# Performance work log

Hardware: AMD Instinct MI355X
Metric: run time of the kernel (lower is better)

## Reference

```python
import jax, jax.numpy as jnp
import numpy as np

DT_MIN, DT_MAX = 1e-3, 0.1
DT_RANK, D_STATE, D_CONV = 64, 16, 4


def setup_inputs() -> dict:
    key = jax.random.key(0)
    ks = jax.random.split(key, 8)
    B, T, Dm = 4, 4096, 1024
    Dn = 2 * Dm  # expand * d_model
    s = lambda k, shape, scale=0.02: (jax.random.normal(k, shape, jnp.float32) * scale)
    return {
        "x": jax.random.normal(ks[0], (B, T, Dm), jnp.float32),
        "W_in": s(ks[1], (2 * Dn, Dm)),
        "conv_w": s(ks[2], (Dn, 1, D_CONV), 0.1),
        "conv_b": jnp.zeros((Dn,), jnp.float32),
        "W_x": s(ks[3], (DT_RANK + 2 * D_STATE, Dn)),
        "W_dt": s(ks[4], (Dn, DT_RANK)),
        "b_dt": jnp.zeros((Dn,), jnp.float32),
        "log_A": jax.random.uniform(ks[5], (Dn, D_STATE), jnp.float32),
        "D_param": jnp.ones((Dn,), jnp.float32),
        "W_out": s(ks[6], (Dm, Dn)),
        "ln_w": jnp.ones((Dm,), jnp.float32),
        "ln_b": jnp.zeros((Dm,), jnp.float32),
    }


def reference(x, W_in, conv_w, conv_b, W_x, W_dt, b_dt, log_A, D_param, W_out, ln_w, ln_b):
    B, T, Dm = x.shape
    Dn = W_dt.shape[0]
    residual = x
    # LayerNorm (biased variance, eps=1e-5, as torch)
    mu = x.mean(-1, keepdims=True)
    var = x.var(-1, keepdims=True)
    xn = (x - mu) / jnp.sqrt(var + 1e-5) * ln_w + ln_b
    # in_proj -> split into x_inner, z
    xz = xn @ W_in.T  # (B,T,2*Dn)
    x_inner, z = jnp.split(xz, 2, axis=-1)
    # causal depthwise conv (torch pads both sides d_conv-1 then slices [:T] == left-pad only)
    xc = jnp.transpose(x_inner, (0, 2, 1))  # (B,Dn,T)
    xc = jax.lax.conv_general_dilated(
        xc, conv_w, window_strides=(1,), padding=[(D_CONV - 1, 0)],
        dimension_numbers=("NCH", "OIH", "NCH"), feature_group_count=Dn)
    xc = xc + conv_b[None, :, None]
    u = jax.nn.silu(jnp.transpose(xc, (0, 2, 1)))  # (B,T,Dn)
    # input-dependent dt, B, C
    xbc = u @ W_x.T
    dt_low, B_ssm, C_ssm = jnp.split(xbc, [DT_RANK, DT_RANK + D_STATE], axis=-1)
    dt = jax.nn.softplus(dt_low @ W_dt.T + b_dt) + DT_MIN
    dt = jnp.clip(dt, DT_MIN, DT_MAX)  # (B,T,Dn)
    A = -jnp.exp(log_A)  # (Dn,N), always negative -> stable
    # selective scan: h_t = exp(dt*A)*h_{t-1} + (dt*u)*B_t ; y_t = <C_t, h_t>
    def step(h, inp):
        dt_t, u_t, B_t, C_t = inp  # (B,Dn),(B,Dn),(B,N),(B,N)
        dA = jnp.exp(dt_t[:, :, None] * A)  # (B,Dn,N)
        h = dA * h + (dt_t * u_t)[:, :, None] * B_t[:, None, :]
        y = jnp.einsum("bdn,bn->bd", h, C_t)
        return h, y

    h0 = jnp.zeros((B, Dn, D_STATE), x.dtype)
    _, ys = jax.lax.scan(
        step, h0,
        (jnp.moveaxis(dt, 1, 0), jnp.moveaxis(u, 1, 0),
         jnp.moveaxis(B_ssm, 1, 0), jnp.moveaxis(C_ssm, 1, 0)))
    y = jnp.moveaxis(ys, 0, 1)  # (B,T,Dn)
    y = y + u * D_param
    y = y * jax.nn.silu(z)
    return y @ W_out.T + residual
```

## Files before the change

kernel.cpp:

```cpp
#include <hip/hip_runtime.h>
#include <cstdint>
#include <cstddef>

#define TT 4096
#define DM 1024
#define DN 2048
#define MROWS 16384
#define NCH 64
#define CHL 64
#define SW 16
#define XBCS 128

typedef unsigned short u16;
typedef u16 ushort8_t __attribute__((ext_vector_type(8)));
typedef u16 ushort4_t __attribute__((ext_vector_type(4)));
typedef short bf16x8 __attribute__((ext_vector_type(8)));
typedef float f32x4 __attribute__((ext_vector_type(4)));

#define EXP2(x) __builtin_amdgcn_exp2f(x)
#define L2E 1.44269504f

__device__ __forceinline__ float bf2f(u16 b) {
  return __uint_as_float(((unsigned int)b) << 16);
}
__device__ __forceinline__ u16 f2bf(float f) {
  unsigned int u = __float_as_uint(f);
  u = u + 0x7FFFu + ((u >> 16) & 1u);
  return (u16)(u >> 16);
}
__device__ __forceinline__ u16 f2h(float f) {
  _Float16 h = (_Float16)f;
  return __builtin_bit_cast(u16, h);
}
__device__ __forceinline__ float h2f(u16 v) {
  return (float)__builtin_bit_cast(_Float16, v);
}

__device__ __forceinline__ void gload_lds16(const void* g, void* l) {
  __builtin_amdgcn_global_load_lds(
      (const __attribute__((address_space(1))) unsigned int*)g,
      (__attribute__((address_space(3))) unsigned int*)l, 16, 0, 0);
}

#define FENCE() asm volatile("" ::: "memory")

__global__ __launch_bounds__(256) void cvt_weights_kernel(
    const float* __restrict__ W_in, u16* __restrict__ W_in_b,
    const float* __restrict__ W_x, u16* __restrict__ W_x_b,
    const float* __restrict__ W_dt, u16* __restrict__ W_dt_b,
    const float* __restrict__ W_out, u16* __restrict__ W_out_b) {
  int b = blockIdx.x, t = threadIdx.x;
  if (b < 4096) {
    int i = b * 256 + t;
    float4 v = ((const float4*)W_in)[i];
    ushort4_t o; o[0] = f2bf(v.x); o[1] = f2bf(v.y); o[2] = f2bf(v.z); o[3] = f2bf(v.w);
    ((ushort4_t*)W_in_b)[i] = o;
  } else if (b < 4352) {
    int i = (b - 4096) * 256 + t;
    int row = i >> 9;
    ushort4_t o;
    if (row < 96) {
      float4 v = ((const float4*)W_x)[i];
      o[0] = f2bf(v.x); o[1] = f2bf(v.y); o[2] = f2bf(v.z); o[3] = f2bf(v.w);
    } else {
      o[0] = 0; o[1] = 0; o[2] = 0; o[3] = 0;
    }
    ((ushort4_t*)W_x_b)[i] = o;
  } else if (b < 4384) {
    int i = (b - 4352) * 256 + t;
    float4 v = ((const float4*)W_dt)[i];
    ushort4_t o; o[0] = f2bf(v.x); o[1] = f2bf(v.y); o[2] = f2bf(v.z); o[3] = f2bf(v.w);
    ((ushort4_t*)W_dt_b)[i] = o;
  } else {
    int i = (b - 4384) * 256 + t;
    float4 v = ((const float4*)W_out)[i];
    ushort4_t o; o[0] = f2bf(v.x); o[1] = f2bf(v.y); o[2] = f2bf(v.z); o[3] = f2bf(v.w);
    ((ushort4_t*)W_out_b)[i] = o;
  }
}

__global__ __launch_bounds__(256) void ln_kernel(const float* __restrict__ x,
    const float* __restrict__ ln_w, const float* __restrict__ ln_b,
    u16* __restrict__ xn) {
  int row = blockIdx.x;
  int tid = threadIdx.x;
  const f32x4* xr = (const f32x4*)(x + (size_t)row * DM);
  f32x4 vv = __builtin_nontemporal_load(&xr[tid]);
  float4 v; v.x = vv[0]; v.y = vv[1]; v.z = vv[2]; v.w = vv[3];
  float s  = v.x + v.y + v.z + v.w;
  float s2 = v.x*v.x + v.y*v.y + v.z*v.z + v.w*v.w;
#pragma unroll
  for (int o = 32; o > 0; o >>= 1) { s += __shfl_down(s, o, 64); s2 += __shfl_down(s2, o, 64); }
  __shared__ float red[2][4];
  __shared__ float mv[2];
  int wid = tid >> 6, lane = tid & 63;
  if (lane == 0) { red[0][wid] = s; red[1][wid] = s2; }
  __syncthreads();
  if (tid == 0) {
    float a  = red[0][0] + red[0][1] + red[0][2] + red[0][3];
    float b2 = red[1][0] + red[1][1] + red[1][2] + red[1][3];
    float mean = a * (1.f / DM);
    float var  = b2 * (1.f / DM) - mean * mean;
    mv[0] = mean; mv[1] = rsqrtf(var + 1e-5f);
  }
  __syncthreads();
  float mean = mv[0], inv = mv[1];
  float4 w = ((const float4*)ln_w)[tid];
  float4 b = ((const float4*)ln_b)[tid];
  ushort4_t o;
  o[0] = f2bf((v.x - mean) * inv * w.x + b.x);
  o[1] = f2bf((v.y - mean) * inv * w.y + b.y);
  o[2] = f2bf((v.z - mean) * inv * w.z + b.z);
  o[3] = f2bf((v.w - mean) * inv * w.w + b.w);
  *(ushort4_t*)(xn + (size_t)row * DM + tid * 4) = o;
}

template<int MODE>
__global__ __launch_bounds__(256) void gemm_mfma_nt(
    const u16* __restrict__ A, int lda,
    const u16* __restrict__ B, int ldb,
    void* __restrict__ Cp, int ldc,
    const float* __restrict__ Res, int K,
    const float* __restrict__ bias, u16* __restrict__ dl_out) {
  __shared__ __align__(16) u16 a_s[128 * 64];
  __shared__ __align__(16) u16 b_s[128 * 64];
  const int tid = threadIdx.x;
  const int w = tid >> 6, l = tid & 63;
  const int wr = w >> 1, wc = w & 1;
  const int nbx = gridDim.x, gy = gridDim.y;
  int lin = blockIdx.y * nbx + blockIdx.x;
  int xcd = lin & 7;
  int m = lin >> 3;
  int bi, bj;
  if (gy >= 8) {
    int njx = gy >> 3;
    bi = m / njx;
    bj = xcd * njx + m % njx;
  } else {
    int cpx = (nbx * gy) >> 3;
    int swz = xcd * cpx + m;
    bi = swz % nbx; bj = swz / nbx;
  }
  const int lrow = l >> 3;
  const int scol = ((l & 7) ^ lrow) * 16;

  f32x4 acc[4][4] = {};

  const int brow = (MODE == 4) ? 0 : bj;
  const u16* Abase = A + (size_t)(bi * 128 + w * 8 + lrow) * lda;
  const u16* Bbase = B + (size_t)(brow * 128 + w * 8 + lrow) * ldb;

  int kbeg = 0, kend = K;
  if constexpr (MODE == 4) { kbeg = bj * (K >> 2); kend = kbeg + (K >> 2); }
  for (int k0 = kbeg; k0 < kend; k0 += 64) {
#pragma unroll
    for (int c = 0; c < 4; c++) {
      const char* ga = (const char*)(Abase + (size_t)(c * 32) * lda + k0) + scol;
      const char* gb = (const char*)(Bbase + (size_t)(c * 32) * ldb + k0) + scol;
      gload_lds16(ga, (char*)a_s + c * 4096 + w * 1024);
      gload_lds16(gb, (char*)b_s + c * 4096 + w * 1024);
    }
    __syncthreads();
#pragma unroll
    for (int kk = 0; kk < 2; kk++) {
      bf16x8 af[4], bfr[4];
#pragma unroll
      for (int m2 = 0; m2 < 4; m2++) {
        int fr = wr * 64 + m2 * 16 + (l & 15);
        int cb = (kk * 64 + ((l >> 4) << 4)) ^ ((fr & 7) << 4);
        af[m2] = *(const bf16x8*)((const char*)a_s + fr * 128 + cb);
      }
#pragma unroll
      for (int n = 0; n < 4; n++) {
        int fr = wc * 64 + n * 16 + (l & 15);
        int cb = (kk * 64 + ((l >> 4) << 4)) ^ ((fr & 7) << 4);
        bfr[n] = *(const bf16x8*)((const char*)b_s + fr * 128 + cb);
      }
#pragma unroll
      for (int m2 = 0; m2 < 4; m2++)
#pragma unroll
        for (int n = 0; n < 4; n++)
          acc[m2][n] = __builtin_amdgcn_mfma_f32_16x16x32_bf16(af[m2], bfr[n], acc[m2][n], 0, 0, 0);
    }
    __syncthreads();
  }
  const int col0 = ((MODE == 4) ? 0 : bj * 128) + wc * 64 + (l & 15);
  const int row0 = bi * 128 + wr * 64 + (l >> 4) * 4;
#pragma unroll
  for (int m2 = 0; m2 < 4; m2++)
#pragma unroll
    for (int n = 0; n < 4; n++) {
      int col = col0 + n * 16;
      float bv = 0.f;
      if constexpr (MODE == 3) bv = bias[col];
#pragma unroll
      for (int r = 0; r < 4; r++) {
        size_t row = (size_t)(row0 + m2 * 16 + r);
        float v = acc[m2][n][r];
        if constexpr (MODE == 0) {
          ((u16*)Cp)[row * ldc + col] = f2bf(v);
        } else if constexpr (MODE == 2) {
          v += __builtin_nontemporal_load(&Res[row * ldc + col]);
          __builtin_nontemporal_store(v, &((float*)Cp)[row * ldc + col]);
        } else if constexpr (MODE == 4) {
          ((float*)Cp)[(size_t)bj * ((size_t)MROWS * 128) + row * ldc + col] = v;
        } else {
          float s = v + bv;
          float sp = __logf(1.f + __expf(s));
          float dtv = fminf(sp + 1e-3f, 0.1f);
          ((u16*)Cp)[row * ldc + col] = f2h(dtv);
        }
      }
    }
}

__global__ __launch_bounds__(256) void xbc_merge(const float* __restrict__ p,
    float* __restrict__ xbc, u16* __restrict__ dl) {
  int i = blockIdx.x * 256 + threadIdx.x;
  const size_t PS = (size_t)MROWS * 128 / 4;
  float4 a = ((const float4*)p)[i];
  float4 b = ((const float4*)p)[i + PS];
  float4 c = ((const float4*)p)[i + 2 * PS];
  float4 d = ((const float4*)p)[i + 3 * PS];
  float4 s;
  s.x = (a.x + b.x) + (c.x + d.x);
  s.y = (a.y + b.y) + (c.y + d.y);
  s.z = (a.z + b.z) + (c.z + d.z);
  s.w = (a.w + b.w) + (c.w + d.w);
  ((float4*)xbc)[i] = s;
  int col = (i & 31) * 4;
  if (col < 64) {
    int row = i >> 5;
    ushort4_t o; o[0] = f2bf(s.x); o[1] = f2bf(s.y); o[2] = f2bf(s.z); o[3] = f2bf(s.w);
    *(ushort4_t*)(dl + (size_t)row * 64 + col) = o;
  }
}

template<int MODE>
__global__ __launch_bounds__(512) void gemm256(
    const u16* __restrict__ A, int lda,
    const u16* __restrict__ B, int ldb,
    void* __restrict__ Cp, int ldc,
    const float* __restrict__ Res, int K) {
  extern __shared__ char smem[];
  const int tid = threadIdx.x;
  const int w = tid >> 6, l = tid & 63;
  const int wm = w >> 2, wn = w & 3;
  const int nbx = gridDim.x, gy = gridDim.y;
  int lin = blockIdx.y * nbx + blockIdx.x;
  int xcd = lin & 7, mm = lin >> 3;
  int bi, bj;
  if (gy >= 8) { int njx = gy >> 3; bi = mm / njx; bj = xcd * njx + mm % njx; }
  else { int cpx = (nbx * gy) >> 3; int swz = xcd * cpx + mm; bi = swz % nbx; bj = swz / nbx; }
  const int lrow = l >> 3;
  const int scol = ((l & 7) ^ lrow) * 16;
  const int l15 = l & 15, lhi = (l >> 4) << 4;
  const u16* aRow = A + (size_t)(bi * 256 + w * 8 + lrow) * lda;
  const u16* bRow = B + (size_t)(bj * 256 + w * 8 + lrow) * ldb;
  char* As = smem;
  char* Bs = smem + 65536;

#define IS_A(s, k) gload_lds16((const char*)(aRow + (size_t)((k) * 64) * lda + (size_t)(s) * 64) + scol, \
                               As + ((((s) & 1)) << 15) + (k) * 8192 + w * 1024)
#define IS_B(s, k) gload_lds16((const char*)(bRow + (size_t)((k) * 64) * ldb + (size_t)(s) * 64) + scol, \
                               Bs + ((((s) & 1)) << 15) + (k) * 8192 + w * 1024)

  f32x4 acc[8][4] = {};
  bf16x8 bf[2][4];
  const int NT = K >> 6;

  IS_B(0, 0); IS_B(0, 1); IS_B(0, 2); IS_B(0, 3);
  IS_A(0, 0); IS_A(0, 2); IS_A(0, 1); IS_A(0, 3);
  IS_B(1, 0); IS_B(1, 1); IS_B(1, 2); IS_B(1, 3); IS_A(1, 0);

#define MFMA8(MLO, KK) do { \
    bf16x8 a0_ = ardA(MLO, KK), a1_ = ardA((MLO) + 1, KK); \
    __builtin_amdgcn_s_setprio(1); \
    _Pragma("unroll") \
    for (int n_ = 0; n_ < 4; n_++) { \
      acc[MLO][n_]       = __builtin_amdgcn_mfma_f32_16x16x32_bf16(a0_, bf[KK][n_], acc[MLO][n_], 0, 0, 0); \
      acc[(MLO) + 1][n_] = __builtin_amdgcn_mfma_f32_16x16x32_bf16(a1_, bf[KK][n_], acc[(MLO) + 1][n_], 0, 0, 0); \
    } \
    __builtin_amdgcn_s_setprio(0); \
  } while (0)

  for (int t = 0; t < NT; ++t) {
    const char* Ab = As + ((t & 1) << 15);
    const char* Bb = Bs + ((t & 1) << 15);
    auto ardA = [&](int m, int kk) {
      int fr = wm * 128 + m * 16 + l15;
      int cb = (kk * 64 + lhi) ^ ((fr & 7) << 4);
      return *(const bf16x8*)(Ab + fr * 128 + cb);
    };
    auto ardB = [&](int n, int kk) {
      int fr = wn * 64 + n * 16 + l15;
      int cb = (kk * 64 + lhi) ^ ((fr & 7) << 4);
      return *(const bf16x8*)(Bb + fr * 128 + cb);
    };
    if (t + 1 < NT) IS_A(t + 1, 2);
    FENCE();
    asm volatile("s_waitcnt vmcnt(8)" ::: "memory");
    __builtin_amdgcn_s_barrier();
    FENCE();
    bf[0][0] = ardB(0, 0); bf[0][1] = ardB(1, 0); bf[0][2] = ardB(2, 0); bf[0][3] = ardB(3, 0);
    MFMA8(0, 0);
    if (t + 1 < NT) IS_A(t + 1, 1);
    MFMA8(2, 0);
    if (t + 1 < NT) IS_A(t + 1, 3);
    bf[1][0] = ardB(0, 1); bf[1][1] = ardB(1, 1); bf[1][2] = ardB(2, 1); bf[1][3] = ardB(3, 1);
    MFMA8(0, 1);
    FENCE();
    __builtin_amdgcn_s_barrier();
    FENCE();
    if (t + 2 < NT) IS_B(t + 2, 0);
    MFMA8(2, 1);
    if (t + 2 < NT) IS_B(t + 2, 1);
    FENCE();
    asm volatile("s_waitcnt vmcnt(10)" ::: "memory");
    __builtin_amdgcn_s_barrier();
    FENCE();
    MFMA8(4, 0);
    if (t + 2 < NT) IS_B(t + 2, 2);
    MFMA8(6, 0);
    if (t + 2 < NT) IS_B(t + 2, 3);
    MFMA8(4, 1);
    if (t + 2 < NT) IS_A(t + 2, 0);
    MFMA8(6, 1);
  }
#undef MFMA8
#undef IS_A
#undef IS_B

  const int col0 = bj * 256 + wn * 64 + l15;
  const int row0 = bi * 256 + wm * 128 + (l >> 4) * 4;
  const bool ntst = (MODE == 0) && (bj >= 8);
#pragma unroll
  for (int m = 0; m < 8; m++)
#pragma unroll
    for (int n = 0; n < 4; n++) {
      int col = col0 + n * 16;
#pragma unroll
      for (int r = 0; r < 4; r++) {
        size_t row = (size_t)(row0 + m * 16 + r);
        float v = acc[m][n][r];
        if constexpr (MODE == 0) {
          u16 bv = f2bf(v);
          if (ntst) __builtin_nontemporal_store(bv, &((u16*)Cp)[row * ldc + col]);
          else      ((u16*)Cp)[row * ldc + col] = bv;
        } else {
          v += __builtin_nontemporal_load(&Res[row * ldc + col]);
          __builtin_nontemporal_store(v, &((float*)Cp)[row * ldc + col]);
        }
      }
    }
}

__global__ __launch_bounds__(256) void conv_silu_kernel(const u16* __restrict__ xz,
    const float* __restrict__ conv_w, const float* __restrict__ conv_b,
    u16* __restrict__ u) {
  size_t gid = (size_t)blockIdx.x * 256 + threadIdx.x;
  int c = (int)(gid & 255);
  size_t i = gid >> 8;
  int t = (int)(i & (TT - 1));
  int d0 = c * 8;
  const u16* base = xz + i * 4096 + d0;
  ushort8_t r0 = *(const ushort8_t*)base;
  ushort8_t r1 = 0, r2 = 0, r3 = 0;
  if (t >= 1) r1 = *(const ushort8_t*)(base - 4096);
  if (t >= 2) r2 = *(const ushort8_t*)(base - 2 * 4096);
  if (t >= 3) r3 = *(const ushort8_t*)(base - 3 * 4096);
  float cbv[8];
  *(float4*)&cbv[0] = *(const float4*)(conv_b + d0);
  *(float4*)&cbv[4] = *(const float4*)(conv_b + d0 + 4);
  ushort8_t o;
#pragma unroll
  for (int j = 0; j < 8; j++) {
    float4 w = *(const float4*)(conv_w + (size_t)(d0 + j) * 4);
    float a = cbv[j] + w.w * bf2f(r0[j]) + w.z * bf2f(r1[j])
            + w.y * bf2f(r2[j]) + w.x * bf2f(r3[j]);
    a = a * __builtin_amdgcn_rcpf(1.f + EXP2(-a * L2E));
    o[j] = f2bf(a);
  }
  *(ushort8_t*)(u + i * 2048 + d0) = o;
}

__global__ __launch_bounds__(256) void scan_part1(u16* u_g,
    const u16* __restrict__ dt_g, const float* __restrict__ xbc,
    const float* __restrict__ log_A, const float* __restrict__ D_param,
    u16* __restrict__ hbuf, float* __restrict__ Sbuf) {
  int d0 = blockIdx.x * 128;
  int c  = blockIdx.y;
  int b  = blockIdx.z;
  int tid = threadIdx.x;
  int w = tid >> 6, l = tid & 63;
  int dl = tid >> 1, q = tid & 1, q8 = q << 3;
  int d = d0 + dl;
  __shared__ __align__(16) u16 u_s[2][SW][128];
  __shared__ __align__(16) u16 dts[2][SW][128];
  __shared__ __align__(16) float bc_s[2][SW][32];

  float A2[8];
  {
    float4 la0 = *(const float4*)(log_A + (size_t)d * 16 + q8);
    float4 la1 = *(const float4*)(log_A + (size_t)d * 16 + q8 + 4);
    A2[0] = -EXP2(la0.x * L2E) * L2E; A2[1] = -EXP2(la0.y * L2E) * L2E;
    A2[2] = -EXP2(la0.z * L2E) * L2E; A2[3] = -EXP2(la0.w * L2E) * L2E;
    A2[4] = -EXP2(la1.x * L2E) * L2E; A2[5] = -EXP2(la1.y * L2E) * L2E;
    A2[6] = -EXP2(la1.z * L2E) * L2E; A2[7] = -EXP2(la1.w * L2E) * L2E;
  }
  float Dp = D_param[d];
  float h[8] = {};
  float sdt = 0.f;
  size_t t0 = (size_t)b * TT + (size_t)c * CHL;
  const int sr = w * 4 + (l >> 4);
  const int sc = (l & 15) * 8;
  u16* up = u_g + t0 * 2048 + d;

#define P1STAGE(wnd, pb) { size_t i0_ = t0 + (size_t)(wnd) * SW;                          \
    gload_lds16(u_g  + (i0_ + sr) * 2048 + d0 + sc, (char*)u_s[pb] + w * 1024);           \
    gload_lds16(dt_g + (i0_ + sr) * 4096 + d0 + sc, (char*)dts[pb] + w * 1024);           \
    if (w < 2) gload_lds16(xbc + (i0_ + w * 8 + (l >> 3)) * XBCS + 64 + (l & 7) * 4,      \
                           (char*)bc_s[pb] + w * 1024); }

  P1STAGE(0, 0);
  for (int wnd = 0; wnd < CHL / SW; wnd++) {
    int pb = wnd & 1;
    __syncthreads();
    if (wnd + 1 < CHL / SW) P1STAGE(wnd + 1, pb ^ 1);
#pragma unroll 4
    for (int tt = 0; tt < SW; tt++) {
      float dtv = h2f(dts[pb][tt][dl]);
      float uv  = bf2f(u_s[pb][tt][dl]);
      sdt += dtv;
      float xin = dtv * uv;
      float yv = q ? 0.f : uv * Dp;
      float4 B0 = *(const float4*)&bc_s[pb][tt][q8];
      float4 B1 = *(const float4*)&bc_s[pb][tt][q8 + 4];
      float4 C0 = *(const float4*)&bc_s[pb][tt][16 + q8];
      float4 C1 = *(const float4*)&bc_s[pb][tt][16 + q8 + 4];
      h[0] = __builtin_fmaf(EXP2(dtv * A2[0]), h[0], xin * B0.x); yv = __builtin_fmaf(h[0], C0.x, yv);
      h[1] = __builtin_fmaf(EXP2(dtv * A2[1]), h[1], xin * B0.y); yv = __builtin_fmaf(h[1], C0.y, yv);
      h[2] = __builtin_fmaf(EXP2(dtv * A2[2]), h[2], xin * B0.z); yv = __builtin_fmaf(h[2], C0.z, yv);
      h[3] = __builtin_fmaf(EXP2(dtv * A2[3]), h[3], xin * B0.w); yv = __builtin_fmaf(h[3], C0.w, yv);
      h[4] = __builtin_fmaf(EXP2(dtv * A2[4]), h[4], xin * B1.x); yv = __builtin_fmaf(h[4], C1.x, yv);
      h[5] = __builtin_fmaf(EXP2(dtv * A2[5]), h[5], xin * B1.y); yv = __builtin_fmaf(h[5], C1.y, yv);
      h[6] = __builtin_fmaf(EXP2(dtv * A2[6]), h[6], xin * B1.z); yv = __builtin_fmaf(h[6], C1.z, yv);
      h[7] = __builtin_fmaf(EXP2(dtv * A2[7]), h[7], xin * B1.w); yv = __builtin_fmaf(h[7], C1.w, yv);
      yv += __shfl_xor(yv, 1, 64);
      if (q == 0) *up = f2h(yv);
      up += 2048;
    }
  }
  u16* hp = hbuf + (((size_t)b * NCH + c) * 16 + q8) * DN + d;
#pragma unroll
  for (int k = 0; k < 8; k++) hp[(size_t)k * DN] = f2h(h[k]);
  if (q == 0) Sbuf[((size_t)b * NCH + c) * DN + d] = sdt;
#undef P1STAGE
}

__global__ __launch_bounds__(256) void scan_combine(const float* __restrict__ log_A,
    const float* __restrict__ Sbuf, u16* __restrict__ hbuf) {
  int idx = blockIdx.x * 256 + threadIdx.x;
  int dd = idx & (DN - 1), n = (idx >> 11) & 15, b = idx >> 15;
  float A2 = -EXP2(log_A[(size_t)dd * 16 + n] * L2E) * L2E;
  float h = 0.f;
#pragma unroll
  for (int c = 0; c < NCH; c++) {
    size_t off = (((size_t)b * NCH + c) * 16 + n) * DN + dd;
    float hl = h2f(hbuf[off]);
    float P = EXP2(A2 * Sbuf[((size_t)b * NCH + c) * DN + dd]);
    hbuf[off] = f2h(h);
    h = hl + P * h;
  }
}

__global__ __launch_bounds__(256) void scan_part2(u16* yl,
    const u16* __restrict__ xz, const float* __restrict__ xbc,
    const u16* __restrict__ dt_g, const float* __restrict__ log_A,
    const u16* __restrict__ hbuf) {
  int d0 = blockIdx.x * 128;
  int c  = blockIdx.y;
  int b  = blockIdx.z;
  int tid = threadIdx.x;
  int w = tid >> 6, l = tid & 63;
  int dl = tid >> 1, q = tid & 1, q8 = q << 3;
  int d = d0 + dl;
  __shared__ __align__(16) u16 yls[2][SW][128];
  __shared__ __align__(16) u16 z_s[2][SW][128];
  __shared__ __align__(16) u16 dts[2][SW][128];
  __shared__ __align__(16) float c_s[2][SW][16];

  float A2[8];
  {
    float4 la0 = *(const float4*)(log_A + (size_t)d * 16 + q8);
    float4 la1 = *(const float4*)(log_A + (size_t)d * 16 + q8 + 4);
    A2[0] = -EXP2(la0.x * L2E) * L2E; A2[1] = -EXP2(la0.y * L2E) * L2E;
    A2[2] = -EXP2(la0.z * L2E) * L2E; A2[3] = -EXP2(la0.w * L2E) * L2E;
    A2[4] = -EXP2(la1.x * L2E) * L2E; A2[5] = -EXP2(la1.y * L2E) * L2E;
    A2[6] = -EXP2(la1.z * L2E) * L2E; A2[7] = -EXP2(la1.w * L2E) * L2E;
  }
  float hs[8];
  {
    const u16* hp = hbuf + (((size_t)b * NCH + c) * 16 + q8) * DN + d;
#pragma unroll
    for (int k = 0; k < 8; k++) hs[k] = h2f(hp[(size_t)k * DN]);
  }
  float cum = 0.f;
  size_t t0 = (size_t)b * TT + (size_t)c * CHL;
  const int sr = w * 4 + (l >> 4);
  const int sc = (l & 15) * 8;
  u16* ylp = yl + t0 * 2048 + d;

#define P2STAGE(wnd, pb) { size_t i0_ = t0 + (size_t)(wnd) * SW;                          \
    gload_lds16(yl   + (i0_ + sr) * 2048 + d0 + sc, (char*)yls[pb] + w * 1024);           \
    gload_lds16(xz   + (i0_ + sr) * 4096 + 2048 + d0 + sc, (char*)z_s[pb] + w * 1024);    \
    gload_lds16(dt_g + (i0_ + sr) * 4096 + d0 + sc, (char*)dts[pb] + w * 1024);           \
    if (w == 0) gload_lds16(xbc + (i0_ + (l >> 2)) * XBCS + 80 + (l & 3) * 4,             \
                            (char*)c_s[pb]); }

  P2STAGE(0, 0);
  for (int wnd = 0; wnd < CHL / SW; wnd++) {
    int pb = wnd & 1;
    __syncthreads();
    if (wnd + 1 < CHL / SW) P2STAGE(wnd + 1, pb ^ 1);
#pragma unroll 4
    for (int tt = 0; tt < SW; tt++) {
      float dtv = h2f(dts[pb][tt][dl]);
      cum += dtv;
      float4 C0 = *(const float4*)&c_s[pb][tt][q8];
      float4 C1 = *(const float4*)&c_s[pb][tt][q8 + 4];
      float yv = C0.x * (EXP2(cum * A2[0]) * hs[0]) + C0.y * (EXP2(cum * A2[1]) * hs[1])
               + C0.z * (EXP2(cum * A2[2]) * hs[2]) + C0.w * (EXP2(cum * A2[3]) * hs[3])
               + C1.x * (EXP2(cum * A2[4]) * hs[4]) + C1.y * (EXP2(cum * A2[5]) * hs[5])
               + C1.z * (EXP2(cum * A2[6]) * hs[6]) + C1.w * (EXP2(cum * A2[7]) * hs[7]);
      if (q == 0) yv += h2f(yls[pb][tt][dl]);
      yv += __shfl_xor(yv, 1, 64);
      float zv = bf2f(z_s[pb][tt][dl]);
      float sig = __builtin_amdgcn_rcpf(1.f + EXP2(-zv * L2E));
      if (q == 0) *ylp = f2bf(yv * zv * sig);
      ylp += 2048;
    }
  }
#undef P2STAGE
}

extern "C" void kernel_launch(void* const* d_in, const int* in_sizes, int n_in,
                              void* d_out, int out_size, void* d_ws, size_t ws_size,
                              hipStream_t stream) {
  const float* x       = (const float*)d_in[0];
  const float* W_in    = (const float*)d_in[1];
  const float* conv_w  = (const float*)d_in[2];
  const float* conv_b  = (const float*)d_in[3];
  const float* W_x     = (const float*)d_in[4];
  const float* W_dt    = (const float*)d_in[5];
  const float* b_dt    = (const float*)d_in[6];
  const float* log_A   = (const float*)d_in[7];
  const float* D_param = (const float*)d_in[8];
  const float* W_out   = (const float*)d_in[9];
  const float* ln_w    = (const float*)d_in[10];
  const float* ln_b    = (const float*)d_in[11];
  float* out = (float*)d_out;

  size_t need = (size_t)MROWS * 4096 * 2 + (size_t)MROWS * DN * 2 + (size_t)MROWS * 96 * 4;
  if (ws_size < need) return;
  u16*   xz  = (u16*)d_ws;
  u16*   u   = xz + (size_t)MROWS * 4096;
  u16*   W_out_b = (u16*)(u + (size_t)MROWS * DN);

  u16*   xn_b    = (u16*)d_out;
  float* xbc_p   = (float*)d_out;
  float* xbc     = (float*)d_out;
  u16*   hbuf    = (u16*)((char*)d_out + (32u << 20));
  u16*   W_in_b  = (u16*)((char*)d_out + (40u << 20));
  float* Sbuf    = (float*)((char*)d_out + (48u << 20));
  u16*   W_x_b   = (u16*)((char*)d_out + (50u << 20));
  u16*   W_dt_b  = (u16*)((char*)d_out + (50u << 20) + (512u << 10));
  u16*   dl_b    = (u16*)((char*)d_out + (51u << 20));

  static int use256 = -1;
  if (use256 < 0) {
    hipError_t e0 = hipFuncSetAttribute(reinterpret_cast<const void*>(&gemm256<0>),
        hipFuncAttributeMaxDynamicSharedMemorySize, 131072);
    hipError_t e2 = hipFuncSetAttribute(reinterpret_cast<const void*>(&gemm256<2>),
        hipFuncAttributeMaxDynamicSharedMemorySize, 131072);
    use256 = (e0 == hipSuccess && e2 == hipSuccess) ? 1 : 0;
  }

  cvt_weights_kernel<<<6432, 256, 0, stream>>>(
      W_in, W_in_b, W_x, W_x_b, W_dt, W_dt_b, W_out, W_out_b);
  ln_kernel<<<MROWS, 256, 0, stream>>>(x, ln_w, ln_b, xn_b);
  if (use256) {
    gemm256<0><<<dim3(MROWS / 256, 4096 / 256), 512, 131072, stream>>>(
        xn_b, DM, W_in_b, DM, xz, 4096, nullptr, DM);
  } else {
    gemm_mfma_nt<0><<<dim3(MROWS / 128, 4096 / 128), 256, 0, stream>>>(
        xn_b, DM, W_in_b, DM, xz, 4096, nullptr, DM, nullptr, nullptr);
  }
  conv_silu_kernel<<<MROWS, 256, 0, stream>>>(xz, conv_w, conv_b, u);
  gemm_mfma_nt<4><<<dim3(MROWS / 128, 4), 256, 0, stream>>>(
      u, DN, W_x_b, DN, xbc_p, XBCS, nullptr, DN, nullptr, nullptr);
  xbc_merge<<<(MROWS * 128 / 4) / 256, 256, 0, stream>>>(xbc_p, xbc, dl_b);
  gemm_mfma_nt<3><<<dim3(MROWS / 128, DN / 128), 256, 0, stream>>>(
      dl_b, 64, W_dt_b, 64, xz, 4096, nullptr, 64, b_dt, nullptr);
  scan_part1<<<dim3(DN / 128, NCH, 4), 256, 0, stream>>>(
      u, xz, xbc, log_A, D_param, hbuf, Sbuf);
  scan_combine<<<4 * DN * 16 / 256, 256, 0, stream>>>(log_A, Sbuf, hbuf);
  scan_part2<<<dim3(DN / 128, NCH, 4), 256, 0, stream>>>(
      u, xz, xbc, xz, log_A, hbuf);
  if (use256) {
    gemm256<2><<<dim3(MROWS / 256, 1024 / 256), 512, 131072, stream>>>(
        u, DN, W_out_b, DN, out, DM, x, DN);
  } else {
    gemm_mfma_nt<2><<<dim3(MROWS / 128, 1024 / 128), 256, 0, stream>>>(
        u, DN, W_out_b, DN, out, DM, x, DN, nullptr, nullptr);
  }
}
```

Baseline: 588.2 us.

## Run 256x256 GEMM with 16 waves, each owning a 64x64 sub-tile

Doubles the gemm256 block from 8 to 16 waves, so each wave computes a 64x64 output sub-tile instead of 128x64. The accumulator and B-fragment register arrays shrink by half, and the global-to-LDS load schedule and waitcnt thresholds are reworked for the new wave count. The aim is more latency hiding per CU. The cost is more barrier traffic per K-step and a changed pipelining depth. The nontemporal store on the upper columns of the in_proj output is also dropped.

```diff
diff --git a/kernel.cpp b/kernel.cpp
--- a/kernel.cpp
+++ b/kernel.cpp
@@ -237,7 +237,7 @@
 }
 
 template<int MODE>
-__global__ __launch_bounds__(512) void gemm256(
+__global__ __launch_bounds__(1024) void gemm256(
     const u16* __restrict__ A, int lda,
     const u16* __restrict__ B, int ldb,
     void* __restrict__ Cp, int ldc,
@@ -260,26 +260,25 @@
   char* As = smem;
   char* Bs = smem + 65536;
 
-#define IS_A(s, k) gload_lds16((const char*)(aRow + (size_t)((k) * 64) * lda + (size_t)(s) * 64) + scol, \
-                               As + ((((s) & 1)) << 15) + (k) * 8192 + w * 1024)
-#define IS_B(s, k) gload_lds16((const char*)(bRow + (size_t)((k) * 64) * ldb + (size_t)(s) * 64) + scol, \
-                               Bs + ((((s) & 1)) << 15) + (k) * 8192 + w * 1024)
-
-  f32x4 acc[8][4] = {};
-  bf16x8 bf[2][4];
+#define IS_A(s, k) gload_lds16((const char*)(aRow + (size_t)((k) * 128) * lda + (size_t)(s) * 64) + scol, \
+                               As + (((s) & 1) << 15) + (k) * 16384 + w * 1024)
+#define IS_B(s, k) gload_lds16((const char*)(bRow + (size_t)((k) * 128) * ldb + (size_t)(s) * 64) + scol, \
+                               Bs + (((s) & 1) << 15) + (k) * 16384 + w * 1024)
+
+  f32x4 acc[4][4] = {};
+  bf16x8 bf[4];
   const int NT = K >> 6;
 
-  IS_B(0, 0); IS_B(0, 1); IS_B(0, 2); IS_B(0, 3);
-  IS_A(0, 0); IS_A(0, 2); IS_A(0, 1); IS_A(0, 3);
-  IS_B(1, 0); IS_B(1, 1); IS_B(1, 2); IS_B(1, 3); IS_A(1, 0);
+  IS_A(0, 0); IS_A(0, 1); IS_B(0, 0); IS_B(0, 1);
+  IS_B(1, 0); IS_B(1, 1);
 
 #define MFMA8(MLO, KK) do { \
     bf16x8 a0_ = ardA(MLO, KK), a1_ = ardA((MLO) + 1, KK); \
     __builtin_amdgcn_s_setprio(1); \
     _Pragma("unroll") \
     for (int n_ = 0; n_ < 4; n_++) { \
-      acc[MLO][n_]       = __builtin_amdgcn_mfma_f32_16x16x32_bf16(a0_, bf[KK][n_], acc[MLO][n_], 0, 0, 0); \
-      acc[(MLO) + 1][n_] = __builtin_amdgcn_mfma_f32_16x16x32_bf16(a1_, bf[KK][n_], acc[(MLO) + 1][n_], 0, 0, 0); \
+      acc[MLO][n_]       = __builtin_amdgcn_mfma_f32_16x16x32_bf16(a0_, bf[n_], acc[MLO][n_], 0, 0, 0); \
+      acc[(MLO) + 1][n_] = __builtin_amdgcn_mfma_f32_16x16x32_bf16(a1_, bf[n_], acc[(MLO) + 1][n_], 0, 0, 0); \
     } \
     __builtin_amdgcn_s_setprio(0); \
   } while (0)
@@ -288,7 +287,7 @@
     const char* Ab = As + ((t & 1) << 15);
     const char* Bb = Bs + ((t & 1) << 15);
     auto ardA = [&](int m, int kk) {
-      int fr = wm * 128 + m * 16 + l15;
+      int fr = wm * 64 + m * 16 + l15;
       int cb = (kk * 64 + lhi) ^ ((fr & 7) << 4);
       return *(const bf16x8*)(Ab + fr * 128 + cb);
     };
@@ -297,45 +296,35 @@
       int cb = (kk * 64 + lhi) ^ ((fr & 7) << 4);
       return *(const bf16x8*)(Bb + fr * 128 + cb);
     };
-    if (t + 1 < NT) IS_A(t + 1, 2);
-    FENCE();
-    asm volatile("s_waitcnt vmcnt(8)" ::: "memory");
+    if (t + 1 < NT) {
+      IS_A(t + 1, 1);
+      FENCE();
+      asm volatile("s_waitcnt vmcnt(3)" ::: "memory");
+    } else {
+      asm volatile("s_waitcnt vmcnt(0)" ::: "memory");
+    }
     __builtin_amdgcn_s_barrier();
     FENCE();
-    bf[0][0] = ardB(0, 0); bf[0][1] = ardB(1, 0); bf[0][2] = ardB(2, 0); bf[0][3] = ardB(3, 0);
+    bf[0] = ardB(0, 0); bf[1] = ardB(1, 0); bf[2] = ardB(2, 0); bf[3] = ardB(3, 0);
     MFMA8(0, 0);
-    if (t + 1 < NT) IS_A(t + 1, 1);
+    if (t + 1 < NT) IS_A(t + 1, 0);
     MFMA8(2, 0);
-    if (t + 1 < NT) IS_A(t + 1, 3);
-    bf[1][0] = ardB(0, 1); bf[1][1] = ardB(1, 1); bf[1][2] = ardB(2, 1); bf[1][3] = ardB(3, 1);
+    bf[0] = ardB(0, 1); bf[1] = ardB(1, 1); bf[2] = ardB(2, 1); bf[3] = ardB(3, 1);
     MFMA8(0, 1);
     FENCE();
     __builtin_amdgcn_s_barrier();
     FENCE();
-    if (t + 2 < NT) IS_B(t + 2, 0);
+    if (t + 2 < NT) { IS_B(t + 2, 0); IS_B(t + 2, 1); }
     MFMA8(2, 1);
-    if (t + 2 < NT) IS_B(t + 2, 1);
-    FENCE();
-    asm volatile("s_waitcnt vmcnt(10)" ::: "memory");
-    __builtin_amdgcn_s_barrier();
-    FENCE();
-    MFMA8(4, 0);
-    if (t + 2 < NT) IS_B(t + 2, 2);
-    MFMA8(6, 0);
-    if (t + 2 < NT) IS_B(t + 2, 3);
-    MFMA8(4, 1);
-    if (t + 2 < NT) IS_A(t + 2, 0);
-    MFMA8(6, 1);
   }
 #undef MFMA8
 #undef IS_A
 #undef IS_B
 
   const int col0 = bj * 256 + wn * 64 + l15;
-  const int row0 = bi * 256 + wm * 128 + (l >> 4) * 4;
-  const bool ntst = (MODE == 0) && (bj >= 8);
-#pragma unroll
-  for (int m = 0; m < 8; m++)
+  const int row0 = bi * 256 + wm * 64 + (l >> 4) * 4;
+#pragma unroll
+  for (int m = 0; m < 4; m++)
 #pragma unroll
     for (int n = 0; n < 4; n++) {
       int col = col0 + n * 16;
@@ -344,9 +333,7 @@
         size_t row = (size_t)(row0 + m * 16 + r);
         float v = acc[m][n][r];
         if constexpr (MODE == 0) {
-          u16 bv = f2bf(v);
-          if (ntst) __builtin_nontemporal_store(bv, &((u16*)Cp)[row * ldc + col]);
-          else      ((u16*)Cp)[row * ldc + col] = bv;
+          ((u16*)Cp)[row * ldc + col] = f2bf(v);
         } else {
           v += __builtin_nontemporal_load(&Res[row * ldc + col]);
           __builtin_nontemporal_store(v, &((float*)Cp)[row * ldc + col]);
@@ -590,7 +577,7 @@
       W_in, W_in_b, W_x, W_x_b, W_dt, W_dt_b, W_out, W_out_b);
   ln_kernel<<<MROWS, 256, 0, stream>>>(x, ln_w, ln_b, xn_b);
   if (use256) {
-    gemm256<0><<<dim3(MROWS / 256, 4096 / 256), 512, 131072, stream>>>(
+    gemm256<0><<<dim3(MROWS / 256, 4096 / 256), 1024, 131072, stream>>>(
         xn_b, DM, W_in_b, DM, xz, 4096, nullptr, DM);
   } else {
     gemm_mfma_nt<0><<<dim3(MROWS / 128, 4096 / 128), 256, 0, stream>>>(
@@ -608,7 +595,7 @@
   scan_part2<<<dim3(DN / 128, NCH, 4), 256, 0, stream>>>(
       u, xz, xbc, xz, log_A, hbuf);
   if (use256) {
-    gemm256<2><<<dim3(MROWS / 256, 1024 / 256), 512, 131072, stream>>>(
+    gemm256<2><<<dim3(MROWS / 256, 1024 / 256), 1024, 131072, stream>>>(
         u, DN, W_out_b, DN, out, DM, x, DN);
   } else {
     gemm_mfma_nt<2><<<dim3(MROWS / 128, 1024 / 128), 256, 0, stream>>>(
```

Result: no change. 595.6 us (+1.2%).
